# Performance work log

Hardware: AMD Instinct MI355X
Metric: run time of the kernel (lower is better)

Reference implementation:

```python
import jax, jax.numpy as jnp
import numpy as np

N_NODES = 100000
N_EDGES = 600000
IN_C, HID, OUT_C = 128, 256, 1

def _glorot(key, shape):
    fan_in, fan_out = shape[1], shape[0]
    lim = np.sqrt(6.0 / (fan_in + fan_out))
    return jax.random.uniform(key, shape, jnp.float32, -lim, lim)

def setup_inputs() -> dict:
    key = jax.random.key(0)
    ks = jax.random.split(key, 12)
    x = jax.random.normal(ks[0], (N_NODES, IN_C), jnp.float32)
    edge_index = jax.random.randint(ks[1], (2, N_EDGES), 0, N_NODES, jnp.int32)
    return {
        "x": x,
        "edge_index": edge_index,
        # SAGEConv1: lin_l (neighbors, with bias), lin_r (root, no bias)
        "W1l": _glorot(ks[2], (HID, IN_C)),
        "b1": jnp.zeros((HID,), jnp.float32),
        "W1r": _glorot(ks[3], (HID, IN_C)),
        # SAGEConv2
        "W2l": _glorot(ks[4], (HID, HID)),
        "b2": jnp.zeros((HID,), jnp.float32),
        "W2r": _glorot(ks[5], (HID, HID)),
        # MLP head: Linear(HID, HID//2) -> ReLU -> Linear(HID//2, OUT_C)
        "Wf1": _glorot(ks[6], (HID // 2, HID)),
        "bf1": jnp.zeros((HID // 2,), jnp.float32),
        "Wf2": _glorot(ks[7], (OUT_C, HID // 2)),
        "bf2": jnp.zeros((OUT_C,), jnp.float32),
    }

def _sage_conv(x, src, dst, Wl, b, Wr, n_nodes):
    # mean-aggregate source-node features into destination nodes
    msgs = x[src]  # [E, F] gather
    sums = jax.ops.segment_sum(msgs, dst, num_segments=n_nodes)
    cnt = jax.ops.segment_sum(jnp.ones((src.shape[0], 1), x.dtype), dst,
                              num_segments=n_nodes)
    mean = sums / jnp.maximum(cnt, 1.0)  # isolated nodes -> 0
    return mean @ Wl.T + b + x @ Wr.T

def reference(x, edge_index, W1l, b1, W1r, W2l, b2, W2r, Wf1, bf1, Wf2, bf2):
    src, dst = edge_index[0], edge_index[1]
    n = x.shape[0]
    h = jax.nn.elu(_sage_conv(x, src, dst, W1l, b1, W1r, n))
    # dropout p=0.3 is identity in eval mode
    h = jax.nn.elu(_sage_conv(h, src, dst, W2l, b2, W2r, n))
    h = jax.nn.relu(h @ Wf1.T + bf1)
    out = h @ Wf2.T + bf2  # [N, 1]
    return jnp.squeeze(out)
```

## Files before the change

kernel.cpp:

```cpp
#include <hip/hip_runtime.h>
#include <hip/hip_bf16.h>

#define NN 100000
#define NE 600000
#define NBLK 98
#define MPAD 100096

typedef __attribute__((ext_vector_type(4))) int   i32x4;
typedef __attribute__((ext_vector_type(4))) float f32x4;

__device__ __forceinline__ float b2f(unsigned short u) {
  unsigned int v = ((unsigned int)u) << 16;
  return __uint_as_float(v);
}
__device__ __forceinline__ unsigned short f2b(float f) {
  __hip_bfloat16 h = __float2bfloat16(f);
  return *reinterpret_cast<unsigned short*>(&h);
}
__device__ __forceinline__ float elu(float v) {
  return v > 0.0f ? v : (expf(v) - 1.0f);
}
__device__ __forceinline__ void gload_lds16(const void* g, void* l) {
  __builtin_amdgcn_global_load_lds(
      (const __attribute__((address_space(1))) void*)g,
      (__attribute__((address_space(3))) void*)l, 16, 0, 0);
}
__device__ __forceinline__ f32x4 mfma16(i32x4 a, i32x4 b, f32x4 c) {
  asm volatile("v_mfma_f32_16x16x32_bf16 %0, %1, %2, %0"
               : "+v"(c) : "v"(a), "v"(b));
  return c;
}


__global__ __launch_bounds__(256) void hist_kernel(
    const int* __restrict__ ei, int* __restrict__ deg) {
  const int* dst = ei + NE;
  int i = blockIdx.x * 256 + threadIdx.x;
  int n = gridDim.x * 256;
  for (int e = i; e < NE; e += n) atomicAdd(&deg[dst[e]], 1);
}

__global__ __launch_bounds__(256) void scan1_kernel(
    const int* __restrict__ deg, int* __restrict__ row, int* __restrict__ aux) {
  __shared__ int sd[256];
  int b = blockIdx.x, t = threadIdx.x;
  int base = b * 1024 + t * 4;
  int v0 = (base + 0 < NN) ? deg[base + 0] : 0;
  int v1 = (base + 1 < NN) ? deg[base + 1] : 0;
  int v2 = (base + 2 < NN) ? deg[base + 2] : 0;
  int v3 = (base + 3 < NN) ? deg[base + 3] : 0;
  int s = v0 + v1 + v2 + v3;
  sd[t] = s;
  __syncthreads();
  for (int off = 1; off < 256; off <<= 1) {
    int tmp = (t >= off) ? sd[t - off] : 0;
    __syncthreads();
    sd[t] += tmp;
    __syncthreads();
  }
  int excl = sd[t] - s;
  if (base + 0 < NN) row[base + 0] = excl;
  if (base + 1 < NN) row[base + 1] = excl + v0;
  if (base + 2 < NN) row[base + 2] = excl + v0 + v1;
  if (base + 3 < NN) row[base + 3] = excl + v0 + v1 + v2;
  if (t == 255) aux[b] = sd[t];
}

__global__ __launch_bounds__(256) void scan2_kernel(int* __restrict__ aux) {
  __shared__ int sd[256];
  int t = threadIdx.x;
  int v = (t < NBLK) ? aux[t] : 0;
  sd[t] = v;
  __syncthreads();
  for (int off = 1; off < 256; off <<= 1) {
    int tmp = (t >= off) ? sd[t - off] : 0;
    __syncthreads();
    sd[t] += tmp;
    __syncthreads();
  }
  if (t < NBLK) aux[t] = sd[t] - v;
}

__global__ __launch_bounds__(256) void scan3_kernel(
    int* __restrict__ row, const int* __restrict__ aux) {
  int i = blockIdx.x * 256 + threadIdx.x;
  if (i < NN) row[i] += aux[i >> 10];
  if (i == 0) row[NN] = NE;
}

__global__ __launch_bounds__(256) void fill_kernel(
    const int* __restrict__ ei, const int* __restrict__ row,
    int* __restrict__ cur, int* __restrict__ eidx) {
  const int* src = ei;
  const int* dst = ei + NE;
  int i = blockIdx.x * 256 + threadIdx.x;
  int n = gridDim.x * 256;
  for (int e = i; e < NE; e += n) {
    int d = dst[e];
    int p = atomicAdd(&cur[d], 1);
    eidx[row[d] + p] = src[e];
  }
}

__global__ __launch_bounds__(256) void conv_x(
    const float* __restrict__ x, unsigned short* __restrict__ A1) {
  int i = blockIdx.x * 256 + threadIdx.x;
  if (i >= NN * 32) return;
  int n = i >> 5, k4 = i & 31;
  float4 v = ((const float4*)(x + (size_t)n * 128))[k4];
  ushort4 o;
  o.x = f2b(v.x); o.y = f2b(v.y); o.z = f2b(v.z); o.w = f2b(v.w);
  ((ushort4*)(A1 + (size_t)n * 256 + 128))[k4] = o;
}

__global__ __launch_bounds__(256) void conv_w(
    const float* __restrict__ W1l, const float* __restrict__ W1r,
    const float* __restrict__ W2l, const float* __restrict__ W2r,
    const float* __restrict__ Wf1,
    unsigned short* __restrict__ W1b, unsigned short* __restrict__ W2b,
    unsigned short* __restrict__ Wf1b) {
  int g = blockIdx.x * 256 + threadIdx.x;
  const float* src;
  unsigned short* dst;
  int j, k, NC;
  if (g < 8192) {
    j = g >> 5; k = (g & 31) * 8; NC = 256; dst = W1b;
    src = (k < 128) ? (W1l + (size_t)j * 128 + k)
                    : (W1r + (size_t)j * 128 + (k - 128));
  } else if (g < 24576) {
    int h = g - 8192; j = h >> 6; k = (h & 63) * 8; NC = 256; dst = W2b;
    src = (k < 256) ? (W2l + (size_t)j * 256 + k)
                    : (W2r + (size_t)j * 256 + (k - 256));
  } else if (g < 28672) {
    int h = g - 24576; j = h >> 5; k = (h & 31) * 8; NC = 128; dst = Wf1b;
    src = Wf1 + (size_t)j * 256 + k;
  } else return;
  float4 v0 = *(const float4*)src;
  float4 v1 = *(const float4*)(src + 4);
  unsigned short o[8] = {f2b(v0.x), f2b(v0.y), f2b(v0.z), f2b(v0.w),
                         f2b(v1.x), f2b(v1.y), f2b(v1.z), f2b(v1.w)};
  size_t off = (size_t)(k >> 5) * (NC * 32) + (j >> 4) * 512 +
               ((k >> 3) & 3) * 128 + (j & 15) * 8;
  *(i32x4*)(dst + off) = *(i32x4*)o;
}

__global__ __launch_bounds__(256) void agg1_csr(
    unsigned short* __restrict__ A1, const int* __restrict__ row,
    const int* __restrict__ eidx) {
  int lane = threadIdx.x & 63;
  int n = (blockIdx.x * 256 + threadIdx.x) >> 6;
  if (n >= NN) return;
  int r0 = row[n], r1 = row[n + 1];
  float ax = 0.f, ay = 0.f;
  int e = r0;
  for (; e + 3 < r1; e += 4) {
    int s0 = eidx[e], s1 = eidx[e + 1], s2 = eidx[e + 2], s3 = eidx[e + 3];
    ushort2 a = ((const ushort2*)(A1 + (size_t)s0 * 256 + 128))[lane];
    ushort2 b = ((const ushort2*)(A1 + (size_t)s1 * 256 + 128))[lane];
    ushort2 c = ((const ushort2*)(A1 + (size_t)s2 * 256 + 128))[lane];
    ushort2 d = ((const ushort2*)(A1 + (size_t)s3 * 256 + 128))[lane];
    ax += (b2f(a.x) + b2f(b.x)) + (b2f(c.x) + b2f(d.x));
    ay += (b2f(a.y) + b2f(b.y)) + (b2f(c.y) + b2f(d.y));
  }
  for (; e < r1; ++e) {
    int s0 = eidx[e];
    ushort2 a = ((const ushort2*)(A1 + (size_t)s0 * 256 + 128))[lane];
    ax += b2f(a.x);
    ay += b2f(a.y);
  }
  float inv = 1.0f / (float)max(r1 - r0, 1);
  ushort2 o;
  o.x = f2b(ax * inv);
  o.y = f2b(ay * inv);
  ((ushort2*)(A1 + (size_t)n * 256))[lane] = o;
}

__global__ __launch_bounds__(256) void agg2_csr(
    unsigned short* __restrict__ A2, const int* __restrict__ row,
    const int* __restrict__ eidx) {
  int lane = threadIdx.x & 63;
  int n = (blockIdx.x * 256 + threadIdx.x) >> 6;
  if (n >= NN) return;
  int r0 = row[n], r1 = row[n + 1];
  float4 acc = make_float4(0.f, 0.f, 0.f, 0.f);
  int e = r0;
  for (; e + 3 < r1; e += 4) {
    int s0 = eidx[e], s1 = eidx[e + 1], s2 = eidx[e + 2], s3 = eidx[e + 3];
    ushort4 a = ((const ushort4*)(A2 + (size_t)s0 * 512 + 256))[lane];
    ushort4 b = ((const ushort4*)(A2 + (size_t)s1 * 512 + 256))[lane];
    ushort4 c = ((const ushort4*)(A2 + (size_t)s2 * 512 + 256))[lane];
    ushort4 d = ((const ushort4*)(A2 + (size_t)s3 * 512 + 256))[lane];
    acc.x += (b2f(a.x) + b2f(b.x)) + (b2f(c.x) + b2f(d.x));
    acc.y += (b2f(a.y) + b2f(b.y)) + (b2f(c.y) + b2f(d.y));
    acc.z += (b2f(a.z) + b2f(b.z)) + (b2f(c.z) + b2f(d.z));
    acc.w += (b2f(a.w) + b2f(b.w)) + (b2f(c.w) + b2f(d.w));
  }
  for (; e < r1; ++e) {
    int s0 = eidx[e];
    ushort4 a = ((const ushort4*)(A2 + (size_t)s0 * 512 + 256))[lane];
    acc.x += b2f(a.x);
    acc.y += b2f(a.y);
    acc.z += b2f(a.z);
    acc.w += b2f(a.w);
  }
  float inv = 1.0f / (float)max(r1 - r0, 1);
  ushort4 o;
  o.x = f2b(acc.x * inv);
  o.y = f2b(acc.y * inv);
  o.z = f2b(acc.z * inv);
  o.w = f2b(acc.w * inv);
  ((ushort4*)(A2 + (size_t)n * 512))[lane] = o;
}

template <int K, int APITCH, int EPI, int AP, int BNC, int HPACK>
__global__ __launch_bounds__(256, 4) void gemm_kernel(
    const unsigned short* __restrict__ A, const unsigned short* __restrict__ Wb,
    const float* __restrict__ bias, const float* __restrict__ w2,
    const float* __restrict__ bf2p,
    unsigned short* __restrict__ Hout, int HPITCH, int HOFF,
    float* __restrict__ out) {
  __shared__ unsigned short lA[2][4096];
  __shared__ unsigned short lB[2][4096];
  int tid = threadIdx.x;
  int w = tid >> 6, lane = tid & 63;
  int lhi = lane >> 4, llo = lane & 15;
  int m0 = blockIdx.x * 128;
  int c0 = blockIdx.y * 128;
  int fb = lane * 8;

  f32x4 acc0[8], acc1[8];
#pragma unroll
  for (int n = 0; n < 8; ++n) { acc0[n] = (f32x4)0.f; acc1[n] = (f32x4)0.f; }

#define STAGE(t)                                                                \
  do {                                                                          \
    int _b = (t) & 1;                                                           \
    _Pragma("unroll")                                                           \
    for (int i = 0; i < 2; ++i) {                                               \
      int c = w * 2 + i;                                                        \
      const unsigned short* ga;                                                 \
      if constexpr (AP) {                                                       \
        ga = A + (size_t)(m0 >> 7) * (128 * K) + (size_t)(t) * 4096 +           \
             c * 512 + lane * 8;                                                \
      } else {                                                                  \
        ga = A + (size_t)(m0 + c * 16 + llo) * APITCH + (t) * 32 + lhi * 8;     \
      }                                                                         \
      gload_lds16(ga, &lA[_b][c * 512]);                                        \
      const unsigned short* gb = Wb + (size_t)(t) * (BNC * 32) +                \
                                 ((c0 >> 4) + c) * 512 + lane * 8;              \
      gload_lds16(gb, &lB[_b][c * 512]);                                        \
    }                                                                           \
  } while (0)

  constexpr int NSTEP = K / 32;
  STAGE(0);
  __builtin_amdgcn_sched_barrier(0);
  asm volatile("s_waitcnt vmcnt(0)" ::: "memory");
  __syncthreads();
  for (int t = 0; t < NSTEP; ++t) {
    if (t + 1 < NSTEP) STAGE(t + 1);
    const unsigned short* la = &lA[t & 1][0];
    const unsigned short* lb = &lB[t & 1][0];
    i32x4 a0 = *(const i32x4*)(la + (w * 2 + 0) * 512 + fb);
    i32x4 a1 = *(const i32x4*)(la + (w * 2 + 1) * 512 + fb);
#pragma unroll
    for (int n = 0; n < 8; ++n) {
      i32x4 b = *(const i32x4*)(lb + n * 512 + fb);
      acc0[n] = mfma16(a0, b, acc0[n]);
      acc1[n] = mfma16(a1, b, acc1[n]);
    }
    __builtin_amdgcn_sched_barrier(0);
    asm volatile("s_waitcnt vmcnt(0)" ::: "memory");
    __syncthreads();
  }
#undef STAGE
  asm volatile("s_nop 7\n\ts_nop 7");

  if constexpr (EPI == 0) {
    float bv[8];
#pragma unroll
    for (int n = 0; n < 8; ++n) bv[n] = bias[c0 + n * 16 + llo];
#pragma unroll
    for (int mi = 0; mi < 2; ++mi) {
#pragma unroll
      for (int n = 0; n < 8; ++n) {
        f32x4 av = mi ? acc1[n] : acc0[n];
#pragma unroll
        for (int r = 0; r < 4; ++r) {
          int R = m0 + (w * 2 + mi) * 16 + lhi * 4 + r;
          float v = elu(av[r] + bv[n]);
          if constexpr (HPACK) {
            int col = c0 + n * 16 + llo;
            size_t off = (size_t)(R >> 7) * 32768 + (col >> 5) * 4096 +
                         ((R >> 4) & 7) * 512 + ((col >> 3) & 3) * 128 +
                         (R & 15) * 8 + (col & 7);
            Hout[off] = f2b(v);
          } else {
            Hout[(size_t)R * HPITCH + HOFF + c0 + n * 16 + llo] = f2b(v);
          }
        }
      }
    }
  } else {
    float b1v[8], w2v[8];
#pragma unroll
    for (int n = 0; n < 8; ++n) {
      b1v[n] = bias[n * 16 + llo];
      w2v[n] = w2[n * 16 + llo];
    }
    float bf2v = bf2p[0];
#pragma unroll
    for (int mi = 0; mi < 2; ++mi) {
#pragma unroll
      for (int r = 0; r < 4; ++r) {
        float s = 0.f;
#pragma unroll
        for (int n = 0; n < 8; ++n) {
          f32x4 av = mi ? acc1[n] : acc0[n];
          s += fmaxf(av[r] + b1v[n], 0.f) * w2v[n];
        }
        s += __shfl_xor(s, 1);
        s += __shfl_xor(s, 2);
        s += __shfl_xor(s, 4);
        s += __shfl_xor(s, 8);
        int R = m0 + (w * 2 + mi) * 16 + lhi * 4 + r;
        if (llo == 0 && R < NN) out[R] = s + bf2v;
      }
    }
  }
}

extern "C" void kernel_launch(void* const* d_in, const int* in_sizes, int n_in,
                              void* d_out, int out_size, void* d_ws, size_t ws_size,
                              hipStream_t stream) {
  const float* x   = (const float*)d_in[0];
  const int*   ei  = (const int*)d_in[1];
  const float* W1l = (const float*)d_in[2];
  const float* b1  = (const float*)d_in[3];
  const float* W1r = (const float*)d_in[4];
  const float* W2l = (const float*)d_in[5];
  const float* b2  = (const float*)d_in[6];
  const float* W2r = (const float*)d_in[7];
  const float* Wf1 = (const float*)d_in[8];
  const float* bf1 = (const float*)d_in[9];
  const float* Wf2 = (const float*)d_in[10];
  const float* bf2 = (const float*)d_in[11];
  float* out = (float*)d_out;

  char* ws = (char*)d_ws;
  size_t o = 0;
  int* deg = (int*)(ws + o); o += 400384;
  int* cur = (int*)(ws + o); o += 400384;
  size_t zero_bytes = o;
  int* row  = (int*)(ws + o); o += 400640;
  int* aux  = (int*)(ws + o); o += 4096;
  int* eidx = (int*)(ws + o); o += 2400000;
  unsigned short* A1 = (unsigned short*)(ws + o); o += (size_t)MPAD * 256 * 2;
  unsigned short* A2 = (unsigned short*)(ws + o); o += (size_t)MPAD * 512 * 2;
  unsigned short* h2 = (unsigned short*)(ws + o); o += (size_t)MPAD * 256 * 2;
  unsigned short* W1b  = (unsigned short*)(ws + o); o += 131072;
  unsigned short* W2b  = (unsigned short*)(ws + o); o += 262144;
  unsigned short* Wf1b = (unsigned short*)(ws + o); o += 65536;

  hipMemsetAsync(d_ws, 0, zero_bytes, stream);

  hist_kernel<<<2048, 256, 0, stream>>>(ei, deg);
  scan1_kernel<<<NBLK, 256, 0, stream>>>(deg, row, aux);
  scan2_kernel<<<1, 256, 0, stream>>>(aux);
  scan3_kernel<<<(NN + 255) / 256, 256, 0, stream>>>(row, aux);
  fill_kernel<<<2048, 256, 0, stream>>>(ei, row, cur, eidx);

  conv_x<<<(NN * 32 + 255) / 256, 256, 0, stream>>>(x, A1);
  conv_w<<<112, 256, 0, stream>>>(W1l, W1r, W2l, W2r, Wf1, W1b, W2b, Wf1b);

  agg1_csr<<<25000, 256, 0, stream>>>(A1, row, eidx);
  gemm_kernel<256, 256, 0, 0, 256, 0><<<dim3(MPAD / 128, 2), 256, 0, stream>>>(
      A1, W1b, b1, nullptr, nullptr, A2, 512, 256, nullptr);
  agg2_csr<<<25000, 256, 0, stream>>>(A2, row, eidx);
  gemm_kernel<512, 512, 0, 0, 256, 1><<<dim3(MPAD / 128, 2), 256, 0, stream>>>(
      A2, W2b, b2, nullptr, nullptr, h2, 0, 0, nullptr);
  gemm_kernel<256, 256, 1, 1, 128, 0><<<dim3(MPAD / 128, 1), 256, 0, stream>>>(
      h2, Wf1b, bf1, Wf2, bf2, nullptr, 0, 0, out);
}
```

Baseline: 286.0 us.

## Widen GEMM tile to full 256 output columns per block

```diff
diff --git a/kernel.cpp b/kernel.cpp
--- a/kernel.cpp
+++ b/kernel.cpp
@@ -212,25 +212,24 @@
   ((ushort4*)(A2 + (size_t)n * 512))[lane] = o;
 }
 
-template <int K, int APITCH, int EPI, int AP, int BNC, int HPACK>
-__global__ __launch_bounds__(256, 4) void gemm_kernel(
+template <int K, int APITCH, int NF, int EPI, int AP, int BNC, int HPACK>
+__global__ __launch_bounds__(256, NF == 16 ? 3 : 4) void gemm_kernel(
     const unsigned short* __restrict__ A, const unsigned short* __restrict__ Wb,
     const float* __restrict__ bias, const float* __restrict__ w2,
     const float* __restrict__ bf2p,
     unsigned short* __restrict__ Hout, int HPITCH, int HOFF,
     float* __restrict__ out) {
   __shared__ unsigned short lA[2][4096];
-  __shared__ unsigned short lB[2][4096];
+  __shared__ unsigned short lB[2][NF * 512];
   int tid = threadIdx.x;
   int w = tid >> 6, lane = tid & 63;
   int lhi = lane >> 4, llo = lane & 15;
   int m0 = blockIdx.x * 128;
-  int c0 = blockIdx.y * 128;
   int fb = lane * 8;
 
-  f32x4 acc0[8], acc1[8];
-#pragma unroll
-  for (int n = 0; n < 8; ++n) { acc0[n] = (f32x4)0.f; acc1[n] = (f32x4)0.f; }
+  f32x4 acc0[NF], acc1[NF];
+#pragma unroll
+  for (int n = 0; n < NF; ++n) { acc0[n] = (f32x4)0.f; acc1[n] = (f32x4)0.f; }
 
 #define STAGE(t)                                                                \
   do {                                                                          \
@@ -246,8 +245,12 @@
         ga = A + (size_t)(m0 + c * 16 + llo) * APITCH + (t) * 32 + lhi * 8;     \
       }                                                                         \
       gload_lds16(ga, &lA[_b][c * 512]);                                        \
+    }                                                                           \
+    _Pragma("unroll")                                                           \
+    for (int i = 0; i < NF / 4; ++i) {                                          \
+      int c = w * (NF / 4) + i;                                                 \
       const unsigned short* gb = Wb + (size_t)(t) * (BNC * 32) +                \
-                                 ((c0 >> 4) + c) * 512 + lane * 8;              \
+                                 c * 512 + lane * 8;                            \
       gload_lds16(gb, &lB[_b][c * 512]);                                        \
     }                                                                           \
   } while (0)
@@ -264,7 +267,7 @@
     i32x4 a0 = *(const i32x4*)(la + (w * 2 + 0) * 512 + fb);
     i32x4 a1 = *(const i32x4*)(la + (w * 2 + 1) * 512 + fb);
 #pragma unroll
-    for (int n = 0; n < 8; ++n) {
+    for (int n = 0; n < NF; ++n) {
       i32x4 b = *(const i32x4*)(lb + n * 512 + fb);
       acc0[n] = mfma16(a0, b, acc0[n]);
       acc1[n] = mfma16(a1, b, acc1[n]);
@@ -277,34 +280,37 @@
   asm volatile("s_nop 7\n\ts_nop 7");
 
   if constexpr (EPI == 0) {
-    float bv[8];
-#pragma unroll
-    for (int n = 0; n < 8; ++n) bv[n] = bias[c0 + n * 16 + llo];
+    float bv[NF];
+#pragma unroll
+    for (int n = 0; n < NF; ++n) bv[n] = bias[n * 16 + llo];
+    int cp[NF];
+#pragma unroll
+    for (int n = 0; n < NF; ++n) {
+      int col = n * 16 + llo;
+      cp[n] = (col >> 5) * 4096 + ((col >> 3) & 3) * 128 + (col & 7);
+    }
+    size_t mb = (size_t)(m0 >> 7) * 32768;
 #pragma unroll
     for (int mi = 0; mi < 2; ++mi) {
 #pragma unroll
-      for (int n = 0; n < 8; ++n) {
+      for (int n = 0; n < NF; ++n) {
         f32x4 av = mi ? acc1[n] : acc0[n];
 #pragma unroll
         for (int r = 0; r < 4; ++r) {
           int R = m0 + (w * 2 + mi) * 16 + lhi * 4 + r;
           float v = elu(av[r] + bv[n]);
           if constexpr (HPACK) {
-            int col = c0 + n * 16 + llo;
-            size_t off = (size_t)(R >> 7) * 32768 + (col >> 5) * 4096 +
-                         ((R >> 4) & 7) * 512 + ((col >> 3) & 3) * 128 +
-                         (R & 15) * 8 + (col & 7);
-            Hout[off] = f2b(v);
+            Hout[mb + cp[n] + (w * 2 + mi) * 512 + (lhi * 4 + r) * 8] = f2b(v);
           } else {
-            Hout[(size_t)R * HPITCH + HOFF + c0 + n * 16 + llo] = f2b(v);
+            Hout[(size_t)R * HPITCH + HOFF + n * 16 + llo] = f2b(v);
           }
         }
       }
     }
   } else {
-    float b1v[8], w2v[8];
-#pragma unroll
-    for (int n = 0; n < 8; ++n) {
+    float b1v[NF], w2v[NF];
+#pragma unroll
+    for (int n = 0; n < NF; ++n) {
       b1v[n] = bias[n * 16 + llo];
       w2v[n] = w2[n * 16 + llo];
     }
@@ -315,7 +321,7 @@
       for (int r = 0; r < 4; ++r) {
         float s = 0.f;
 #pragma unroll
-        for (int n = 0; n < 8; ++n) {
+        for (int n = 0; n < NF; ++n) {
           f32x4 av = mi ? acc1[n] : acc0[n];
           s += fmaxf(av[r] + b1v[n], 0.f) * w2v[n];
         }
@@ -374,11 +380,11 @@
   conv_w<<<112, 256, 0, stream>>>(W1l, W1r, W2l, W2r, Wf1, W1b, W2b, Wf1b);
 
   agg1_csr<<<25000, 256, 0, stream>>>(A1, row, eidx);
-  gemm_kernel<256, 256, 0, 0, 256, 0><<<dim3(MPAD / 128, 2), 256, 0, stream>>>(
+  gemm_kernel<256, 256, 16, 0, 0, 256, 0><<<MPAD / 128, 256, 0, stream>>>(
       A1, W1b, b1, nullptr, nullptr, A2, 512, 256, nullptr);
   agg2_csr<<<25000, 256, 0, stream>>>(A2, row, eidx);
-  gemm_kernel<512, 512, 0, 0, 256, 1><<<dim3(MPAD / 128, 2), 256, 0, stream>>>(
+  gemm_kernel<512, 512, 16, 0, 0, 256, 1><<<MPAD / 128, 256, 0, stream>>>(
       A2, W2b, b2, nullptr, nullptr, h2, 0, 0, nullptr);
-  gemm_kernel<256, 256, 1, 1, 128, 0><<<dim3(MPAD / 128, 1), 256, 0, stream>>>(
+  gemm_kernel<256, 256, 8, 1, 1, 128, 0><<<MPAD / 128, 256, 0, stream>>>(
       h2, Wf1b, bf1, Wf2, bf2, nullptr, 0, 0, out);
 }
```

After: 294.9 us. 1.03x slower.
